# Performance work log

Measured on AMD Instinct MI355X. Metric: run time of the kernel, lower is better.

Reference implementation:

```python
import jax, jax.numpy as jnp
import numpy as np

B, S, H, D = 2, 2048, 16, 128


def setup_inputs() -> dict:
    key = jax.random.key(0)
    kq, kk, kv = jax.random.split(key, 3)
    return {
        "query": jax.random.normal(kq, (B, S, H, D), dtype=jnp.float32),
        "key": jax.random.normal(kk, (B, S, H, D), dtype=jnp.float32),
        "value": jax.random.normal(kv, (B, S, H, D), dtype=jnp.float32),
    }


def reference(query, key, value):
    # Single-device semantics of HybridAttention: the Ulysses all-to-alls are
    # resharding collectives (identity at world_size=1); the ring flash-attn
    # computes standard causal scaled-dot-product attention over the full seq.
    d = query.shape[-1]
    scale = 1.0 / jnp.sqrt(jnp.asarray(d, dtype=query.dtype))
    # [b, h, q, k]
    scores = jnp.einsum("bqhd,bkhd->bhqk", query, key) * scale
    s = query.shape[1]
    causal_mask = jnp.tril(jnp.ones((s, s), dtype=bool))  # [q, k]
    scores = jnp.where(causal_mask[None, None], scores, jnp.finfo(scores.dtype).min)
    probs = jax.nn.softmax(scores, axis=-1)
    out = jnp.einsum("bhqk,bkhd->bqhd", probs, value)
    return out
```

## Files before the change

kernel.cpp:

```cpp
#include <hip/hip_runtime.h>
#include <hip/hip_bf16.h>

constexpr int Bc = 2, Sc = 2048, Hc = 16, Dc = 128;
constexpr int RS = Hc * Dc;
constexpr float SCALE2 = 0.08838834764831845f * 1.4426950408889634f;

constexpr int QBLK = 128;
constexpr int KVBLK = 32;
constexpr int NW = 8;
constexpr int NQB = Sc / QBLK;
constexpr int KPAD = Dc + 8;
constexpr int VPAD = KVBLK;
constexpr int PPAD = KVBLK + 8;

typedef __attribute__((ext_vector_type(8))) short bf16x8;
typedef __attribute__((ext_vector_type(4))) float f32x4;

__device__ __forceinline__ unsigned short f2b(float f) {
  return __builtin_bit_cast(unsigned short, __float2bfloat16(f));
}

__global__ __launch_bounds__(512, 4)
void fa_fwd(const float* __restrict__ Q, const float* __restrict__ K,
            const float* __restrict__ V, float* __restrict__ O) {
  __shared__ unsigned short Klds[2][KVBLK][KPAD];
  __shared__ unsigned short Vt[2][Dc][VPAD];
  __shared__ unsigned short Plds[NW][16][PPAD];

  const int tid = threadIdx.x;
  const int wid = tid >> 6;
  const int lane = tid & 63;
  const int lq = lane & 15;
  const int g = lane >> 4;

  const int n = blockIdx.x;
  int qblk, bh;
  if (n < 256) { qblk = n & 15;        bh = n >> 4; }
  else         { qblk = 15 - (n & 15); bh = 16 + ((n - 256) >> 4); }
  const int b = bh >> 4;
  const int h = bh & 15;

  const int q0 = qblk * QBLK;
  const int qw = q0 + wid * 16;

  const size_t base = (size_t)b * Sc * RS + (size_t)h * Dc;
  const float* Qp = Q + base;
  const float* Kp = K + base;
  const float* Vp = V + base;
  float* Op = O + base;

  bf16x8 qf[4];
  {
    const float* qrow = Qp + (size_t)(qw + lq) * RS + 8 * g;
    #pragma unroll
    for (int c = 0; c < 4; ++c) {
      float4 f0 = *(const float4*)(qrow + 32 * c);
      float4 f1 = *(const float4*)(qrow + 32 * c + 4);
      bf16x8 v;
      v[0] = (short)f2b(f0.x * SCALE2); v[1] = (short)f2b(f0.y * SCALE2);
      v[2] = (short)f2b(f0.z * SCALE2); v[3] = (short)f2b(f0.w * SCALE2);
      v[4] = (short)f2b(f1.x * SCALE2); v[5] = (short)f2b(f1.y * SCALE2);
      v[6] = (short)f2b(f1.z * SCALE2); v[7] = (short)f2b(f1.w * SCALE2);
      qf[c] = v;
    }
  }

  f32x4 acc[8];
  #pragma unroll
  for (int dc = 0; dc < 8; ++dc) acc[dc] = f32x4{0.f, 0.f, 0.f, 0.f};
  float l_r[4] = {0.f, 0.f, 0.f, 0.f};

  const int nkv = (q0 + QBLK) / KVBLK;

  const int krow = tid >> 3;
  const int kseg = tid & 7;
  const int vt_ = tid & 255;
  const int vrow = vt_ & 31;
  const int vseg = vt_ >> 5;

  float4 sreg[4];
  auto issue = [&](int kv0) {
    if (wid < 4) {
      const float4* ks = (const float4*)(Kp + (size_t)(kv0 + krow) * RS + kseg * 16);
      sreg[0] = ks[0]; sreg[1] = ks[1]; sreg[2] = ks[2]; sreg[3] = ks[3];
    } else {
      const float4* vs = (const float4*)(Vp + (size_t)(kv0 + vrow) * RS + vseg * 16);
      sreg[0] = vs[0]; sreg[1] = vs[1]; sreg[2] = vs[2]; sreg[3] = vs[3];
    }
  };
  auto commit = [&](int buf) {
    if (wid < 4) {
      const float* kf = (const float*)sreg;
      bf16x8 w0, w1;
      #pragma unroll
      for (int e = 0; e < 8; ++e) { w0[e] = (short)f2b(kf[e]); w1[e] = (short)f2b(kf[8 + e]); }
      *(bf16x8*)&Klds[buf][krow][kseg * 16] = w0;
      *(bf16x8*)&Klds[buf][krow][kseg * 16 + 8] = w1;
    } else {
      const float* vf = (const float*)sreg;
      #pragma unroll
      for (int e = 0; e < 16; ++e) Vt[buf][vseg * 16 + e][vrow] = f2b(vf[e]);
    }
  };

  issue(0);
  commit(0);
  __syncthreads();

  for (int kb = 0; kb < nkv; ++kb) {
    const int kv0 = kb * KVBLK;
    const int p = kb & 1;
    const bool pf = (kb + 1 < nkv);

    if (pf) issue(kv0 + KVBLK);

    const bool dead = (kv0 > qw + 15);
    if (!dead) {
      f32x4 s0 = {0.f, 0.f, 0.f, 0.f}, s1 = {0.f, 0.f, 0.f, 0.f};
      #pragma unroll
      for (int c = 0; c < 4; ++c) {
        bf16x8 k0 = *(const bf16x8*)&Klds[p][lq][32 * c + 8 * g];
        bf16x8 k1 = *(const bf16x8*)&Klds[p][16 + lq][32 * c + 8 * g];
        s0 = __builtin_amdgcn_mfma_f32_16x16x32_bf16(qf[c], k0, s0, 0, 0, 0);
        s1 = __builtin_amdgcn_mfma_f32_16x16x32_bf16(qf[c], k1, s1, 0, 0, 0);
      }

      bf16x8 vfr[8];
      #pragma unroll
      for (int dc = 0; dc < 8; ++dc)
        vfr[dc] = *(const bf16x8*)&Vt[p][16 * dc + lq][8 * g];

      const bool nomask = (kv0 + KVBLK - 1) <= qw;
      #pragma unroll
      for (int r = 0; r < 4; ++r) {
        float a = s0[r], c2 = s1[r];
        if (!nomask) {
          const int qrow = qw + 4 * g + r;
          a  = (kv0 + lq      > qrow) ? -1e30f : a;
          c2 = (kv0 + 16 + lq > qrow) ? -1e30f : c2;
        }
        const float p0 = __builtin_amdgcn_exp2f(a);
        const float p1 = __builtin_amdgcn_exp2f(c2);
        Plds[wid][4 * g + r][lq] = f2b(p0);
        Plds[wid][4 * g + r][16 + lq] = f2b(p1);
        l_r[r] += p0 + p1;
      }

      const bf16x8 pa = *(const bf16x8*)&Plds[wid][lq][8 * g];
      #pragma unroll
      for (int dc = 0; dc < 8; ++dc)
        acc[dc] = __builtin_amdgcn_mfma_f32_16x16x32_bf16(pa, vfr[dc], acc[dc], 0, 0, 0);
    }

    if (pf) commit(p ^ 1);
    __syncthreads();
  }

  float inv[4];
  #pragma unroll
  for (int r = 0; r < 4; ++r) {
    float l = l_r[r];
    #pragma unroll
    for (int o = 8; o >= 1; o >>= 1) l += __shfl_xor(l, o);
    inv[r] = 1.0f / l;
  }
  float* orow = Op + (size_t)(qw + 4 * g) * RS + lq;
  #pragma unroll
  for (int dc = 0; dc < 8; ++dc) {
    #pragma unroll
    for (int r = 0; r < 4; ++r)
      orow[(size_t)r * RS + 16 * dc] = acc[dc][r] * inv[r];
  }
}

extern "C" void kernel_launch(void* const* d_in, const int* in_sizes, int n_in,
                              void* d_out, int out_size, void* d_ws, size_t ws_size,
                              hipStream_t stream) {
  const float* Q = (const float*)d_in[0];
  const float* K = (const float*)d_in[1];
  const float* V = (const float*)d_in[2];
  float* O = (float*)d_out;
  fa_fwd<<<dim3(NQB * Bc * Hc), dim3(512), 0, stream>>>(Q, K, V, O);
}
```

Measured before the change: 94.25 us.

## Software-pipeline PV MFMA one iteration behind QK and remap block order

```diff
diff --git a/kernel.cpp b/kernel.cpp
--- a/kernel.cpp
+++ b/kernel.cpp
@@ -34,9 +34,9 @@
   const int g = lane >> 4;
 
   const int n = blockIdx.x;
-  int qblk, bh;
-  if (n < 256) { qblk = n & 15;        bh = n >> 4; }
-  else         { qblk = 15 - (n & 15); bh = 16 + ((n - 256) >> 4); }
+  const int bh = n & 31;
+  const int a = (n >> 5) & 7;
+  const int qblk = (n < 256) ? a : 15 - a;
   const int b = bh >> 4;
   const int h = bh & 15;
 
@@ -107,6 +107,10 @@
   commit(0);
   __syncthreads();
 
+  bf16x8 paP;
+  bf16x8 vfrP[8];
+  bool havePrev = false;
+
   for (int kb = 0; kb < nkv; ++kb) {
     const int kv0 = kb * KVBLK;
     const int p = kb & 1;
@@ -115,8 +119,16 @@
     if (pf) issue(kv0 + KVBLK);
 
     const bool dead = (kv0 > qw + 15);
+
+    __builtin_amdgcn_s_setprio(1);
+    if (havePrev) {
+      #pragma unroll
+      for (int dc = 0; dc < 8; ++dc)
+        acc[dc] = __builtin_amdgcn_mfma_f32_16x16x32_bf16(paP, vfrP[dc], acc[dc], 0, 0, 0);
+    }
+
+    f32x4 s0 = {0.f, 0.f, 0.f, 0.f}, s1 = {0.f, 0.f, 0.f, 0.f};
     if (!dead) {
-      f32x4 s0 = {0.f, 0.f, 0.f, 0.f}, s1 = {0.f, 0.f, 0.f, 0.f};
       #pragma unroll
       for (int c = 0; c < 4; ++c) {
         bf16x8 k0 = *(const bf16x8*)&Klds[p][lq][32 * c + 8 * g];
@@ -124,36 +136,42 @@
         s0 = __builtin_amdgcn_mfma_f32_16x16x32_bf16(qf[c], k0, s0, 0, 0, 0);
         s1 = __builtin_amdgcn_mfma_f32_16x16x32_bf16(qf[c], k1, s1, 0, 0, 0);
       }
-
-      bf16x8 vfr[8];
+    }
+    __builtin_amdgcn_s_setprio(0);
+
+    if (!dead) {
       #pragma unroll
       for (int dc = 0; dc < 8; ++dc)
-        vfr[dc] = *(const bf16x8*)&Vt[p][16 * dc + lq][8 * g];
+        vfrP[dc] = *(const bf16x8*)&Vt[p][16 * dc + lq][8 * g];
 
       const bool nomask = (kv0 + KVBLK - 1) <= qw;
       #pragma unroll
       for (int r = 0; r < 4; ++r) {
-        float a = s0[r], c2 = s1[r];
+        float sa = s0[r], sb = s1[r];
         if (!nomask) {
           const int qrow = qw + 4 * g + r;
-          a  = (kv0 + lq      > qrow) ? -1e30f : a;
-          c2 = (kv0 + 16 + lq > qrow) ? -1e30f : c2;
+          sa = (kv0 + lq      > qrow) ? -1e30f : sa;
+          sb = (kv0 + 16 + lq > qrow) ? -1e30f : sb;
         }
-        const float p0 = __builtin_amdgcn_exp2f(a);
-        const float p1 = __builtin_amdgcn_exp2f(c2);
+        const float p0 = __builtin_amdgcn_exp2f(sa);
+        const float p1 = __builtin_amdgcn_exp2f(sb);
         Plds[wid][4 * g + r][lq] = f2b(p0);
         Plds[wid][4 * g + r][16 + lq] = f2b(p1);
         l_r[r] += p0 + p1;
       }
 
-      const bf16x8 pa = *(const bf16x8*)&Plds[wid][lq][8 * g];
-      #pragma unroll
-      for (int dc = 0; dc < 8; ++dc)
-        acc[dc] = __builtin_amdgcn_mfma_f32_16x16x32_bf16(pa, vfr[dc], acc[dc], 0, 0, 0);
-    }
+      paP = *(const bf16x8*)&Plds[wid][lq][8 * g];
+    }
+    havePrev = !dead;
 
     if (pf) commit(p ^ 1);
     __syncthreads();
+  }
+
+  if (havePrev) {
+    #pragma unroll
+    for (int dc = 0; dc < 8; ++dc)
+      acc[dc] = __builtin_amdgcn_mfma_f32_16x16x32_bf16(paP, vfrP[dc], acc[dc], 0, 0, 0);
   }
 
   float inv[4];
```

New measurement: 118.3 us. 25.5% more time.

## Swizzle K/V LDS layouts, keep P in registers via shuffles, remap block order

Applied to the files above, without the earlier changes.

```diff
diff --git a/kernel.cpp b/kernel.cpp
--- a/kernel.cpp
+++ b/kernel.cpp
@@ -7,25 +7,25 @@
 
 constexpr int QBLK = 128;
 constexpr int KVBLK = 32;
-constexpr int NW = 8;
 constexpr int NQB = Sc / QBLK;
-constexpr int KPAD = Dc + 8;
-constexpr int VPAD = KVBLK;
-constexpr int PPAD = KVBLK + 8;
+constexpr int VROW = 40;
 
 typedef __attribute__((ext_vector_type(8))) short bf16x8;
 typedef __attribute__((ext_vector_type(4))) float f32x4;
+typedef __attribute__((ext_vector_type(4))) unsigned int u32x4;
 
 __device__ __forceinline__ unsigned short f2b(float f) {
   return __builtin_bit_cast(unsigned short, __float2bfloat16(f));
+}
+__device__ __forceinline__ unsigned int pk2(float lo, float hi) {
+  return (unsigned int)f2b(lo) | ((unsigned int)f2b(hi) << 16);
 }
 
 __global__ __launch_bounds__(512, 4)
 void fa_fwd(const float* __restrict__ Q, const float* __restrict__ K,
             const float* __restrict__ V, float* __restrict__ O) {
-  __shared__ unsigned short Klds[2][KVBLK][KPAD];
-  __shared__ unsigned short Vt[2][Dc][VPAD];
-  __shared__ unsigned short Plds[NW][16][PPAD];
+  __shared__ unsigned short Kl[2][KVBLK * Dc];
+  __shared__ unsigned short Vt[2][Dc * VROW];
 
   const int tid = threadIdx.x;
   const int wid = tid >> 6;
@@ -34,9 +34,9 @@
   const int g = lane >> 4;
 
   const int n = blockIdx.x;
-  int qblk, bh;
-  if (n < 256) { qblk = n & 15;        bh = n >> 4; }
-  else         { qblk = 15 - (n & 15); bh = 16 + ((n - 256) >> 4); }
+  const int bh = n & 31;
+  const int a = (n >> 5) & 7;
+  const int qblk = (n < 256) ? a : 15 - a;
   const int b = bh >> 4;
   const int h = bh & 15;
 
@@ -68,15 +68,15 @@
   f32x4 acc[8];
   #pragma unroll
   for (int dc = 0; dc < 8; ++dc) acc[dc] = f32x4{0.f, 0.f, 0.f, 0.f};
-  float l_r[4] = {0.f, 0.f, 0.f, 0.f};
+  float lsum = 0.f;
 
   const int nkv = (q0 + QBLK) / KVBLK;
 
   const int krow = tid >> 3;
   const int kseg = tid & 7;
-  const int vt_ = tid & 255;
-  const int vrow = vt_ & 31;
-  const int vseg = vt_ >> 5;
+  const int t2 = tid & 255;
+  const int vm = t2 >> 4;
+  const int vc = t2 & 15;
 
   float4 sreg[4];
   auto issue = [&](int kv0) {
@@ -84,8 +84,10 @@
       const float4* ks = (const float4*)(Kp + (size_t)(kv0 + krow) * RS + kseg * 16);
       sreg[0] = ks[0]; sreg[1] = ks[1]; sreg[2] = ks[2]; sreg[3] = ks[3];
     } else {
-      const float4* vs = (const float4*)(Vp + (size_t)(kv0 + vrow) * RS + vseg * 16);
-      sreg[0] = vs[0]; sreg[1] = vs[1]; sreg[2] = vs[2]; sreg[3] = vs[3];
+      const float* ve = Vp + (size_t)(kv0 + 2 * vm) * RS + vc * 8;
+      const float* vo = ve + RS;
+      sreg[0] = ((const float4*)ve)[0]; sreg[1] = ((const float4*)ve)[1];
+      sreg[2] = ((const float4*)vo)[0]; sreg[3] = ((const float4*)vo)[1];
     }
   };
   auto commit = [&](int buf) {
@@ -94,12 +96,19 @@
       bf16x8 w0, w1;
       #pragma unroll
       for (int e = 0; e < 8; ++e) { w0[e] = (short)f2b(kf[e]); w1[e] = (short)f2b(kf[8 + e]); }
-      *(bf16x8*)&Klds[buf][krow][kseg * 16] = w0;
-      *(bf16x8*)&Klds[buf][krow][kseg * 16 + 8] = w1;
+      const int sw = krow & 7;
+      *(bf16x8*)&Kl[buf][krow * 128 + ((2 * kseg) ^ sw) * 8] = w0;
+      *(bf16x8*)&Kl[buf][krow * 128 + ((2 * kseg + 1) ^ sw) * 8] = w1;
     } else {
-      const float* vf = (const float*)sreg;
-      #pragma unroll
-      for (int e = 0; e < 16; ++e) Vt[buf][vseg * 16 + e][vrow] = f2b(vf[e]);
+      const float* ef = (const float*)&sreg[0];
+      const float* of = (const float*)&sreg[2];
+      #pragma unroll
+      for (int i = 0; i < 8; ++i) {
+        const int d = 8 * vc + i;
+        const unsigned int w = pk2(ef[i], of[i]);
+        const int slot = (vm >> 2) ^ ((d >> 3) & 3);
+        *(unsigned int*)&Vt[buf][d * VROW + slot * 8 + (vm & 3) * 2] = w;
+      }
     }
   };
 
@@ -119,34 +128,51 @@
       f32x4 s0 = {0.f, 0.f, 0.f, 0.f}, s1 = {0.f, 0.f, 0.f, 0.f};
       #pragma unroll
       for (int c = 0; c < 4; ++c) {
-        bf16x8 k0 = *(const bf16x8*)&Klds[p][lq][32 * c + 8 * g];
-        bf16x8 k1 = *(const bf16x8*)&Klds[p][16 + lq][32 * c + 8 * g];
-        s0 = __builtin_amdgcn_mfma_f32_16x16x32_bf16(qf[c], k0, s0, 0, 0, 0);
-        s1 = __builtin_amdgcn_mfma_f32_16x16x32_bf16(qf[c], k1, s1, 0, 0, 0);
+        const int slotK = (4 * c + g) ^ (lq & 7);
+        bf16x8 k0 = *(const bf16x8*)&Kl[p][lq * 128 + slotK * 8];
+        bf16x8 k1 = *(const bf16x8*)&Kl[p][(16 + lq) * 128 + slotK * 8];
+        s0 = __builtin_amdgcn_mfma_f32_16x16x32_bf16(k0, qf[c], s0, 0, 0, 0);
+        s1 = __builtin_amdgcn_mfma_f32_16x16x32_bf16(k1, qf[c], s1, 0, 0, 0);
       }
 
       bf16x8 vfr[8];
       #pragma unroll
-      for (int dc = 0; dc < 8; ++dc)
-        vfr[dc] = *(const bf16x8*)&Vt[p][16 * dc + lq][8 * g];
+      for (int dc = 0; dc < 8; ++dc) {
+        const int d = 16 * dc + lq;
+        const int slotV = g ^ ((2 * dc + (lq >> 3)) & 3);
+        vfr[dc] = *(const bf16x8*)&Vt[p][d * VROW + slotV * 8];
+      }
 
       const bool nomask = (kv0 + KVBLK - 1) <= qw;
+      float p0[4], p1[4];
       #pragma unroll
       for (int r = 0; r < 4; ++r) {
-        float a = s0[r], c2 = s1[r];
+        float sa = s0[r], sb = s1[r];
         if (!nomask) {
-          const int qrow = qw + 4 * g + r;
-          a  = (kv0 + lq      > qrow) ? -1e30f : a;
-          c2 = (kv0 + 16 + lq > qrow) ? -1e30f : c2;
+          const int q = qw + lq;
+          sa = (kv0 + 4 * g + r      > q) ? -1e30f : sa;
+          sb = (kv0 + 16 + 4 * g + r > q) ? -1e30f : sb;
         }
-        const float p0 = __builtin_amdgcn_exp2f(a);
-        const float p1 = __builtin_amdgcn_exp2f(c2);
-        Plds[wid][4 * g + r][lq] = f2b(p0);
-        Plds[wid][4 * g + r][16 + lq] = f2b(p1);
-        l_r[r] += p0 + p1;
-      }
-
-      const bf16x8 pa = *(const bf16x8*)&Plds[wid][lq][8 * g];
+        p0[r] = __builtin_amdgcn_exp2f(sa);
+        p1[r] = __builtin_amdgcn_exp2f(sb);
+        lsum += p0[r] + p1[r];
+      }
+
+      const unsigned int a0 = pk2(p0[0], p0[1]);
+      const unsigned int a1 = pk2(p0[2], p0[3]);
+      const unsigned int b0 = pk2(p1[0], p1[1]);
+      const unsigned int b1 = pk2(p1[2], p1[3]);
+      const int sl = lq + ((g & 1) << 5);
+      const int sh = sl + 16;
+      const unsigned int xa0 = __shfl((int)a0, sl), xb0 = __shfl((int)b0, sl);
+      const unsigned int xa1 = __shfl((int)a1, sl), xb1 = __shfl((int)b1, sl);
+      const unsigned int ya0 = __shfl((int)a0, sh), yb0 = __shfl((int)b0, sh);
+      const unsigned int ya1 = __shfl((int)a1, sh), yb1 = __shfl((int)b1, sh);
+      const bool tlo = (g < 2);
+      u32x4 pw = { tlo ? xa0 : xb0, tlo ? xa1 : xb1,
+                   tlo ? ya0 : yb0, tlo ? ya1 : yb1 };
+      const bf16x8 pa = __builtin_bit_cast(bf16x8, pw);
+
       #pragma unroll
       for (int dc = 0; dc < 8; ++dc)
         acc[dc] = __builtin_amdgcn_mfma_f32_16x16x32_bf16(pa, vfr[dc], acc[dc], 0, 0, 0);
@@ -156,14 +182,12 @@
     __syncthreads();
   }
 
+  lsum += __shfl_xor(lsum, 16);
+  lsum += __shfl_xor(lsum, 32);
   float inv[4];
   #pragma unroll
-  for (int r = 0; r < 4; ++r) {
-    float l = l_r[r];
-    #pragma unroll
-    for (int o = 8; o >= 1; o >>= 1) l += __shfl_xor(l, o);
-    inv[r] = 1.0f / l;
-  }
+  for (int r = 0; r < 4; ++r)
+    inv[r] = 1.0f / __shfl(lsum, 4 * g + r);
   float* orow = Op + (size_t)(qw + 4 * g) * RS + lq;
   #pragma unroll
   for (int dc = 0; dc < 8; ++dc) {
```

Result: slower. 191.9 us (+103.6%).
